# Optimization experiments

Measured on AMD Instinct MI355X. Metric: run time of the kernel, lower is better.

Reference implementation:

```python
import jax, jax.numpy as jnp
import numpy as np

D_MODEL = 1024
N_HEADS = 16
D_K = D_MODEL // N_HEADS


def _glorot(key, fan_in, fan_out):
    limit = np.sqrt(6.0 / (fan_in + fan_out)).astype(np.float32)
    return jax.random.uniform(key, (fan_in, fan_out), jnp.float32, -limit, limit)


def setup_inputs() -> dict:
    key = jax.random.key(0)
    kx, kq, kk, kv = jax.random.split(key, 4)
    x = jax.random.normal(kx, (2, 2048, D_MODEL), jnp.float32)
    Wq = _glorot(kq, D_MODEL, D_MODEL)
    Wk = _glorot(kk, D_MODEL, D_MODEL)
    Wv = _glorot(kv, D_MODEL, D_MODEL)
    bq = jnp.zeros((D_MODEL,), jnp.float32)
    bk = jnp.zeros((D_MODEL,), jnp.float32)
    bv = jnp.zeros((D_MODEL,), jnp.float32)
    return {"x": x, "Wq": Wq, "bq": bq, "Wk": Wk, "bk": bk, "Wv": Wv, "bv": bv}


def reference(x, Wq, bq, Wk, bk, Wv, bv):
    B, S, _ = x.shape
    # QKV projections (Dense layers with bias)
    q = (x @ Wq + bq).reshape(B, S, N_HEADS, D_K).transpose(0, 2, 1, 3)  # [B,H,S,Dk]
    k = (x @ Wk + bk).reshape(B, S, N_HEADS, D_K).transpose(0, 2, 1, 3)
    v = (x @ Wv + bv).reshape(B, S, N_HEADS, D_K).transpose(0, 2, 1, 3)
    # raw exp-based softmax (NO max subtraction, per original module)
    scores = jnp.einsum('bhqd,bhkd->bhqk', q, k) / np.sqrt(D_K).astype(np.float32)
    scores = jnp.exp(scores)
    attn = scores / (jnp.sum(scores, axis=-1, keepdims=True) + 1e-8)
    context = jnp.einsum('bhqk,bhkd->bhqd', attn, v)  # [B,H,S,Dk]
    return context.transpose(0, 2, 1, 3).reshape(B, S, N_HEADS * D_K)
```

## Files before the change

### kernel.cpp

```cpp
#include <hip/hip_runtime.h>
#include <hip/hip_bf16.h>
#include <stdint.h>

typedef __bf16 bf16x8 __attribute__((ext_vector_type(8)));
typedef __bf16 bf16x4 __attribute__((ext_vector_type(4)));
typedef float  f32x4  __attribute__((ext_vector_type(4)));
typedef short  s16x4  __attribute__((ext_vector_type(4)));
typedef unsigned short u16_t;

#define MFMA(a, b, c)   __builtin_amdgcn_mfma_f32_16x16x32_bf16((a), (b), (c), 0, 0, 0)
#define MFMA16(a, b, c) __builtin_amdgcn_mfma_f32_16x16x16bf16_1k((a), (b), (c), 0, 0, 0)

__device__ __forceinline__ void cp16(const void* g, void* l) {
  __builtin_amdgcn_global_load_lds(
      (const __attribute__((address_space(1))) unsigned int*)g,
      (__attribute__((address_space(3))) unsigned int*)l, 16, 0, 0);
}

__global__ __launch_bounds__(256) void k_prep(const float* __restrict__ x,
                                              const float* __restrict__ W0,
                                              const float* __restrict__ W1,
                                              const float* __restrict__ W2,
                                              u16_t* __restrict__ xb,
                                              u16_t* __restrict__ Wt) {
  __shared__ u16_t T[64][65];
  int bx = blockIdx.x, t = threadIdx.x;
  if (bx < 4096) {
    int i = bx * 256 + t;
    float4 f = ((const float4*)x)[i];
    bf16x4 o = {(__bf16)f.x, (__bf16)f.y, (__bf16)f.z, (__bf16)f.w};
    *(bf16x4*)&xb[(size_t)i * 4] = o;
    return;
  }
  int j = bx - 4096;
  int nx = j & 15, ny = (j >> 4) & 15, z = j >> 8;
  const float* W = z == 0 ? W0 : (z == 1 ? W1 : W2);
  int k0 = ny * 64, n0 = nx * 64;
#pragma unroll
  for (int i = 0; i < 16; i++) {
    int e = i * 256 + t, r = e >> 6, c = e & 63;
    __bf16 hv = (__bf16)W[(size_t)(k0 + r) * 1024 + n0 + c];
    T[r][c] = *(u16_t*)&hv;
  }
  __syncthreads();
  size_t base = ((size_t)z * 1024 + n0) * 1024 + k0;
#pragma unroll
  for (int i = 0; i < 16; i++) {
    int e = i * 256 + t, r = e >> 6, c = e & 63;
    Wt[base + (size_t)r * 1024 + c] = T[c][r];
  }
}

__global__ __launch_bounds__(256) void k_gemm_qkv(
    const u16_t* __restrict__ A, const u16_t* __restrict__ Bt,
    const float* __restrict__ bq, const float* __restrict__ bk,
    const float* __restrict__ bv,
    u16_t* __restrict__ Qo, u16_t* __restrict__ Ko, u16_t* __restrict__ Vo) {
  __shared__ u16_t As[128 * 32];
  __shared__ u16_t Bs[128 * 32];
  const int tid = threadIdx.x, lane = tid & 63, wv = tid >> 6;
  const int quad = lane >> 4, col = lane & 15;
  const int wm = wv >> 1, wn = wv & 1;
  const int tn = blockIdx.x * 128, tm = blockIdx.y * 128;
  f32x4 acc[4][4] = {};

  const int c0 = wv * 2;
  const int srow = lane >> 2;
  const int spc = lane & 3;

  for (int kk = 0; kk < 1024; kk += 32) {
#pragma unroll
    for (int i = 0; i < 2; i++) {
      int c = c0 + i;
      int m = c * 16 + srow;
      int lch = spc ^ ((m >> 1) & 3);
      cp16(A + (size_t)(tm + m) * 1024 + kk + lch * 8, As + c * 512 + lane * 8);
      cp16(Bt + (size_t)(tn + m) * 1024 + kk + lch * 8, Bs + c * 512 + lane * 8);
    }
    __syncthreads();
    bf16x8 af[4], bfv[4];
#pragma unroll
    for (int mt = 0; mt < 4; mt++) {
      int row = wm * 64 + mt * 16 + col;
      af[mt] = *(const bf16x8*)&As[row * 32 + (quad ^ ((row >> 1) & 3)) * 8];
    }
#pragma unroll
    for (int nt = 0; nt < 4; nt++) {
      int row = wn * 64 + nt * 16 + col;
      bfv[nt] = *(const bf16x8*)&Bs[row * 32 + (quad ^ ((row >> 1) & 3)) * 8];
    }
#pragma unroll
    for (int mt = 0; mt < 4; mt++)
#pragma unroll
      for (int nt = 0; nt < 4; nt++)
        acc[mt][nt] = MFMA(af[mt], bfv[nt], acc[mt][nt]);
    __syncthreads();
  }

  const int mat = tn >> 10;
  const float* bias = mat == 0 ? bq : (mat == 1 ? bk : bv);
  if (mat == 2) {
#pragma unroll
    for (int nt = 0; nt < 4; nt++) {
      int gn = tn + wn * 64 + nt * 16 + col;
      int d = gn & 1023, h = d >> 6, dk = d & 63;
      float bb = bias[d];
#pragma unroll
      for (int mt = 0; mt < 4; mt++) {
        int gm = tm + wm * 64 + mt * 16 + quad * 4;
        int b = gm >> 11, s = gm & 2047;
        bf16x4 pk4;
#pragma unroll
        for (int r = 0; r < 4; r++) pk4[r] = (__bf16)(acc[mt][nt][r] + bb);
        *(bf16x4*)&Vo[((size_t)((b * 16 + h) * 64 + dk)) * 2048 + s] = pk4;
      }
    }
  } else {
    u16_t* O = mat == 0 ? Qo : Ko;
    const float scl = mat == 0 ? 0.18033688011112042f : 1.0f;
#pragma unroll
    for (int nt = 0; nt < 4; nt++) {
      int gn = tn + wn * 64 + nt * 16 + col;
      int d = gn & 1023, h = d >> 6, dk = d & 63;
      float bb = bias[d];
#pragma unroll
      for (int mt = 0; mt < 4; mt++) {
#pragma unroll
        for (int r = 0; r < 4; r++) {
          int gm = tm + wm * 64 + mt * 16 + quad * 4 + r;
          int b = gm >> 11, s = gm & 2047;
          __bf16 hv = (__bf16)((acc[mt][nt][r] + bb) * scl);
          O[((size_t)((b * 16 + h) * 2048 + s)) * 64 + dk] = *(u16_t*)&hv;
        }
      }
    }
  }
}

__global__ __launch_bounds__(256, 4) void k_attn(const u16_t* __restrict__ Q,
                                                 const u16_t* __restrict__ K,
                                                 const u16_t* __restrict__ Vt,
                                                 float* __restrict__ out) {
  __shared__ u16_t smem[20480];
  u16_t* Qs  = smem;
  u16_t* Ksb = smem + 4096;
  u16_t* Vsb = smem + 12288;
  const int tid = threadIdx.x, lane = tid & 63, wv = tid >> 6;
  const int quad = lane >> 4, col = lane & 15;
  const int qh = wv >> 1, kh = wv & 1;
  const int qt = blockIdx.x, bh = blockIdx.y;
  const int b = bh >> 4, h = bh & 15;
  const int r8 = lane >> 3, c8 = lane & 7;

  const u16_t* Qg = Q + ((size_t)bh * 2048 + qt * 64) * 64;
  const u16_t* Kg = K + (size_t)bh * 2048 * 64;
  const u16_t* Vg = Vt + (size_t)bh * 64 * 2048;

#pragma unroll
  for (int i = 0; i < 2; i++) {
    int c = wv * 2 + i;
    int row = c * 8 + r8;
    int lch = c8 ^ r8;
    cp16(Qg + (size_t)row * 64 + lch * 8, Qs + c * 512 + lane * 8);
    cp16(Kg + (size_t)row * 64 + lch * 8, Ksb + c * 512 + lane * 8);
    cp16(Vg + (size_t)row * 2048 + lch * 8, Vsb + c * 512 + lane * 8);
  }
  __syncthreads();

  bf16x8 qf[2][2];
#pragma unroll
  for (int nt = 0; nt < 2; nt++)
#pragma unroll
    for (int ks = 0; ks < 2; ks++) {
      int row = qh * 32 + nt * 16 + col;
      qf[nt][ks] = *(const bf16x8*)&Qs[row * 64 + (((ks * 4 + quad) ^ (row & 7)) * 8)];
    }

  const short one_bf = (short)0x3F80;
  s16x4 ones4 = {one_bf, one_bf, one_bf, one_bf};

  f32x4 ao[2][4] = {};
  f32x4 dn[2] = {};

  for (int kt = 0; kt < 32; kt++) {
    const int cur = kt & 1;
    const u16_t* Kc = Ksb + cur * 4096;
    const u16_t* Vc = Vsb + cur * 4096;
    if (kt + 1 < 32) {
      u16_t* Kn = Ksb + (cur ^ 1) * 4096;
      u16_t* Vn = Vsb + (cur ^ 1) * 4096;
#pragma unroll
      for (int i = 0; i < 2; i++) {
        int c = wv * 2 + i;
        int row = c * 8 + r8;
        int lch = c8 ^ r8;
        cp16(Kg + (size_t)(kt + 1) * 4096 + (size_t)row * 64 + lch * 8,
             Kn + c * 512 + lane * 8);
        cp16(Vg + (size_t)row * 2048 + (kt + 1) * 64 + lch * 8,
             Vn + c * 512 + lane * 8);
      }
    }

    f32x4 sc[2][2] = {};
#pragma unroll
    for (int ks = 0; ks < 2; ks++) {
      bf16x8 kf[2];
#pragma unroll
      for (int mt = 0; mt < 2; mt++) {
        int row = kh * 32 + mt * 16 + col;
        kf[mt] = *(const bf16x8*)&Kc[row * 64 + (((ks * 4 + quad) ^ (row & 7)) * 8)];
      }
#pragma unroll
      for (int mt = 0; mt < 2; mt++)
#pragma unroll
        for (int nt = 0; nt < 2; nt++)
          sc[mt][nt] = MFMA(kf[mt], qf[nt][ks], sc[mt][nt]);
    }

    s16x4 pf[2][2];
#pragma unroll
    for (int mt = 0; mt < 2; mt++)
#pragma unroll
      for (int nt = 0; nt < 2; nt++) {
#pragma unroll
        for (int r = 0; r < 4; r++) {
          __bf16 e = (__bf16)__builtin_amdgcn_exp2f(sc[mt][nt][r]);
          pf[mt][nt][r] = *(short*)&e;
        }
        dn[nt] = MFMA16(pf[mt][nt], ones4, dn[nt]);
      }

#pragma unroll
    for (int mt = 0; mt < 2; mt++) {
#pragma unroll
      for (int dt = 0; dt < 4; dt++) {
        int row = dt * 16 + col;
        int c = kh * 4 + mt * 2 + (quad >> 1);
        int addr = row * 64 + ((c ^ (row & 7)) * 8) + (quad & 1) * 4;
        s16x4 vf = *(const s16x4*)&Vc[addr];
#pragma unroll
        for (int nt = 0; nt < 2; nt++)
          ao[nt][dt] = MFMA16(pf[mt][nt], vf, ao[nt][dt]);
      }
    }
    __syncthreads();
  }

  float* red = (float*)(smem + 4096);
  const int rb = (qh * 64 + lane) * 41;
  if (kh == 1) {
#pragma unroll
    for (int nt = 0; nt < 2; nt++) {
#pragma unroll
      for (int dt = 0; dt < 4; dt++)
#pragma unroll
        for (int r = 0; r < 4; r++)
          red[rb + (nt * 4 + dt) * 4 + r] = ao[nt][dt][r];
#pragma unroll
      for (int r = 0; r < 4; r++)
        red[rb + 32 + nt * 4 + r] = dn[nt][r];
    }
  }
  __syncthreads();
  if (kh == 0) {
#pragma unroll
    for (int nt = 0; nt < 2; nt++) {
      float dsum[4];
#pragma unroll
      for (int r = 0; r < 4; r++)
        dsum[r] = dn[nt][r] + red[rb + 32 + nt * 4 + r] + 1e-8f;
#pragma unroll
      for (int dt = 0; dt < 4; dt++) {
#pragma unroll
        for (int r = 0; r < 4; r++) {
          float v = (ao[nt][dt][r] + red[rb + (nt * 4 + dt) * 4 + r]) / dsum[r];
          int s = qt * 64 + qh * 32 + nt * 16 + quad * 4 + r;
          out[((size_t)b * 2048 + s) * 1024 + h * 64 + dt * 16 + col] = v;
        }
      }
    }
  }
}

extern "C" void kernel_launch(void* const* d_in, const int* in_sizes, int n_in,
                              void* d_out, int out_size, void* d_ws, size_t ws_size,
                              hipStream_t stream) {
  const float* x  = (const float*)d_in[0];
  const float* Wq = (const float*)d_in[1];
  const float* bq = (const float*)d_in[2];
  const float* Wk = (const float*)d_in[3];
  const float* bk = (const float*)d_in[4];
  const float* Wv = (const float*)d_in[5];
  const float* bv = (const float*)d_in[6];
  float* out = (float*)d_out;

  char* ws = (char*)d_ws;
  u16_t* xb  = (u16_t*)(ws);
  u16_t* Wt  = (u16_t*)(ws + 8388608);
  u16_t* Qb  = (u16_t*)(ws + 14680064);
  u16_t* Kb  = (u16_t*)(ws + 23068672);
  u16_t* Vtb = (u16_t*)(ws + 31457280);

  hipLaunchKernelGGL(k_prep, dim3(4864), dim3(256), 0, stream, x, Wq, Wk, Wv, xb, Wt);
  hipLaunchKernelGGL(k_gemm_qkv, dim3(24, 32), dim3(256), 0, stream,
                     xb, Wt, bq, bk, bv, Qb, Kb, Vtb);
  hipLaunchKernelGGL(k_attn, dim3(32, 32), dim3(256), 0, stream, Qb, Kb, Vtb, out);
}
```

Before: 170.7 us.

## Shrink attention blocks to 32 queries with two waves and smaller KV tiles

The attention kernel now uses 128-thread blocks, each handling 32 query rows with two waves that split each 32-key tile, instead of 256-thread blocks handling 64 queries. The grid doubles to 2048 blocks and LDS per block drops to 16 KB. Q fragments are loaded straight from global memory rather than staged through LDS, and the K/V tiles are half-sized with a new swizzle. The aim is more blocks and waves resident per CU and better load balance. In exchange, every K/V tile is read from global memory by twice as many blocks, and there are twice as many loop iterations and barriers.

```diff
diff --git a/kernel.cpp b/kernel.cpp
--- a/kernel.cpp
+++ b/kernel.cpp
@@ -137,44 +137,38 @@
   }
 }
 
-__global__ __launch_bounds__(256, 4) void k_attn(const u16_t* __restrict__ Q,
+__global__ __launch_bounds__(128, 4) void k_attn(const u16_t* __restrict__ Q,
                                                  const u16_t* __restrict__ K,
                                                  const u16_t* __restrict__ Vt,
                                                  float* __restrict__ out) {
-  __shared__ u16_t smem[20480];
-  u16_t* Qs  = smem;
-  u16_t* Ksb = smem + 4096;
-  u16_t* Vsb = smem + 12288;
-  const int tid = threadIdx.x, lane = tid & 63, wv = tid >> 6;
+  __shared__ u16_t smem[8192];
+  u16_t* Ksb = smem;
+  u16_t* Vsb = smem + 4096;
+  const int tid = threadIdx.x, lane = tid & 63, kh = tid >> 6;
   const int quad = lane >> 4, col = lane & 15;
-  const int qh = wv >> 1, kh = wv & 1;
   const int qt = blockIdx.x, bh = blockIdx.y;
   const int b = bh >> 4, h = bh & 15;
-  const int r8 = lane >> 3, c8 = lane & 7;
-
-  const u16_t* Qg = Q + ((size_t)bh * 2048 + qt * 64) * 64;
+
+  const u16_t* Qg = Q + ((size_t)bh * 2048 + qt * 32) * 64;
   const u16_t* Kg = K + (size_t)bh * 2048 * 64;
   const u16_t* Vg = Vt + (size_t)bh * 64 * 2048;
 
-#pragma unroll
-  for (int i = 0; i < 2; i++) {
-    int c = wv * 2 + i;
-    int row = c * 8 + r8;
-    int lch = c8 ^ r8;
-    cp16(Qg + (size_t)row * 64 + lch * 8, Qs + c * 512 + lane * 8);
-    cp16(Kg + (size_t)row * 64 + lch * 8, Ksb + c * 512 + lane * 8);
-    cp16(Vg + (size_t)row * 2048 + lch * 8, Vsb + c * 512 + lane * 8);
-  }
-  __syncthreads();
+  const int krow = lane >> 3, kch = (lane & 7) ^ (lane >> 3);
+  const int vrow = lane >> 2, vch = (lane & 3) ^ ((lane >> 3) & 3);
+
+#pragma unroll
+  for (int j = 0; j < 2; j++) {
+    int sl = kh * 2 + j;
+    cp16(Kg + (size_t)(sl * 8 + krow) * 64 + kch * 8, Ksb + sl * 512 + lane * 8);
+    cp16(Vg + (size_t)(sl * 16 + vrow) * 2048 + vch * 8, Vsb + sl * 512 + lane * 8);
+  }
 
   bf16x8 qf[2][2];
 #pragma unroll
   for (int nt = 0; nt < 2; nt++)
 #pragma unroll
-    for (int ks = 0; ks < 2; ks++) {
-      int row = qh * 32 + nt * 16 + col;
-      qf[nt][ks] = *(const bf16x8*)&Qs[row * 64 + (((ks * 4 + quad) ^ (row & 7)) * 8)];
-    }
+    for (int ks = 0; ks < 2; ks++)
+      qf[nt][ks] = *(const bf16x8*)&Qg[(size_t)(nt * 16 + col) * 64 + ks * 32 + quad * 8];
 
   const short one_bf = (short)0x3F80;
   s16x4 ones4 = {one_bf, one_bf, one_bf, one_bf};
@@ -182,72 +176,60 @@
   f32x4 ao[2][4] = {};
   f32x4 dn[2] = {};
 
-  for (int kt = 0; kt < 32; kt++) {
+  const int vpch = (kh * 2 + (quad >> 1)) ^ ((col >> 1) & 3);
+  __syncthreads();
+
+  for (int kt = 0; kt < 64; kt++) {
     const int cur = kt & 1;
-    const u16_t* Kc = Ksb + cur * 4096;
-    const u16_t* Vc = Vsb + cur * 4096;
-    if (kt + 1 < 32) {
-      u16_t* Kn = Ksb + (cur ^ 1) * 4096;
-      u16_t* Vn = Vsb + (cur ^ 1) * 4096;
-#pragma unroll
-      for (int i = 0; i < 2; i++) {
-        int c = wv * 2 + i;
-        int row = c * 8 + r8;
-        int lch = c8 ^ r8;
-        cp16(Kg + (size_t)(kt + 1) * 4096 + (size_t)row * 64 + lch * 8,
-             Kn + c * 512 + lane * 8);
-        cp16(Vg + (size_t)row * 2048 + (kt + 1) * 64 + lch * 8,
-             Vn + c * 512 + lane * 8);
-      }
-    }
-
-    f32x4 sc[2][2] = {};
+    const u16_t* Kc = Ksb + cur * 2048;
+    const u16_t* Vc = Vsb + cur * 2048;
+    if (kt + 1 < 64) {
+      u16_t* Kn = Ksb + (cur ^ 1) * 2048;
+      u16_t* Vn = Vsb + (cur ^ 1) * 2048;
+#pragma unroll
+      for (int j = 0; j < 2; j++) {
+        int sl = kh * 2 + j;
+        cp16(Kg + (size_t)((kt + 1) * 32 + sl * 8 + krow) * 64 + kch * 8,
+             Kn + sl * 512 + lane * 8);
+        cp16(Vg + (size_t)(sl * 16 + vrow) * 2048 + (kt + 1) * 32 + vch * 8,
+             Vn + sl * 512 + lane * 8);
+      }
+    }
+
+    f32x4 sc[2] = {};
 #pragma unroll
     for (int ks = 0; ks < 2; ks++) {
-      bf16x8 kf[2];
-#pragma unroll
-      for (int mt = 0; mt < 2; mt++) {
-        int row = kh * 32 + mt * 16 + col;
-        kf[mt] = *(const bf16x8*)&Kc[row * 64 + (((ks * 4 + quad) ^ (row & 7)) * 8)];
-      }
-#pragma unroll
-      for (int mt = 0; mt < 2; mt++)
-#pragma unroll
-        for (int nt = 0; nt < 2; nt++)
-          sc[mt][nt] = MFMA(kf[mt], qf[nt][ks], sc[mt][nt]);
-    }
-
-    s16x4 pf[2][2];
-#pragma unroll
-    for (int mt = 0; mt < 2; mt++)
-#pragma unroll
-      for (int nt = 0; nt < 2; nt++) {
-#pragma unroll
-        for (int r = 0; r < 4; r++) {
-          __bf16 e = (__bf16)__builtin_amdgcn_exp2f(sc[mt][nt][r]);
-          pf[mt][nt][r] = *(short*)&e;
-        }
-        dn[nt] = MFMA16(pf[mt][nt], ones4, dn[nt]);
-      }
-
-#pragma unroll
-    for (int mt = 0; mt < 2; mt++) {
-#pragma unroll
-      for (int dt = 0; dt < 4; dt++) {
-        int row = dt * 16 + col;
-        int c = kh * 4 + mt * 2 + (quad >> 1);
-        int addr = row * 64 + ((c ^ (row & 7)) * 8) + (quad & 1) * 4;
-        s16x4 vf = *(const s16x4*)&Vc[addr];
-#pragma unroll
-        for (int nt = 0; nt < 2; nt++)
-          ao[nt][dt] = MFMA16(pf[mt][nt], vf, ao[nt][dt]);
-      }
+      int row = kh * 16 + col;
+      bf16x8 kf = *(const bf16x8*)&Kc[row * 64 + (((ks * 4 + quad) ^ (col & 7)) * 8)];
+#pragma unroll
+      for (int nt = 0; nt < 2; nt++)
+        sc[nt] = MFMA(kf, qf[nt][ks], sc[nt]);
+    }
+
+    s16x4 pf[2];
+#pragma unroll
+    for (int nt = 0; nt < 2; nt++) {
+#pragma unroll
+      for (int r = 0; r < 4; r++) {
+        __bf16 e = (__bf16)__builtin_amdgcn_exp2f(sc[nt][r]);
+        pf[nt][r] = *(short*)&e;
+      }
+      dn[nt] = MFMA16(pf[nt], ones4, dn[nt]);
+    }
+
+#pragma unroll
+    for (int dt = 0; dt < 4; dt++) {
+      int d = dt * 16 + col;
+      s16x4 vf = *(const s16x4*)&Vc[d * 32 + vpch * 8 + (quad & 1) * 4];
+#pragma unroll
+      for (int nt = 0; nt < 2; nt++)
+        ao[nt][dt] = MFMA16(pf[nt], vf, ao[nt][dt]);
     }
     __syncthreads();
   }
 
-  float* red = (float*)(smem + 4096);
-  const int rb = (qh * 64 + lane) * 41;
+  float* red = (float*)smem;
+  const int rb = lane * 41;
   if (kh == 1) {
 #pragma unroll
     for (int nt = 0; nt < 2; nt++) {
@@ -274,7 +256,7 @@
 #pragma unroll
         for (int r = 0; r < 4; r++) {
           float v = (ao[nt][dt][r] + red[rb + (nt * 4 + dt) * 4 + r]) / dsum[r];
-          int s = qt * 64 + qh * 32 + nt * 16 + quad * 4 + r;
+          int s = qt * 32 + nt * 16 + quad * 4 + r;
           out[((size_t)b * 2048 + s) * 1024 + h * 64 + dt * 16 + col] = v;
         }
       }
@@ -304,5 +286,5 @@
   hipLaunchKernelGGL(k_prep, dim3(4864), dim3(256), 0, stream, x, Wq, Wk, Wv, xb, Wt);
   hipLaunchKernelGGL(k_gemm_qkv, dim3(24, 32), dim3(256), 0, stream,
                      xb, Wt, bq, bk, bv, Qb, Kb, Vtb);
-  hipLaunchKernelGGL(k_attn, dim3(32, 32), dim3(256), 0, stream, Qb, Kb, Vtb, out);
-}
+  hipLaunchKernelGGL(k_attn, dim3(64, 32), dim3(128), 0, stream, Qb, Kb, Vtb, out);
+}
```

Result: slower. 184.0 us (+7.8%).

## Restructure attention into two-wave blocks with per-wave private K/V pipelines

Applied to the files above, without the earlier changes.

The attention kernel now uses 128-thread blocks with two waves. Each wave covers all 64 query rows and half of the key range (1024 keys), and streams its own K/V tiles into private LDS double buffers. This removes the block-wide __syncthreads inside the key loop, replacing it with explicit vmcnt waits. Q fragments are loaded straight from global memory into registers, the grid is flattened with a remapped block index for L2 locality, and the V tile layout and swizzle change to 32-key tiles. The cost is more accumulator registers per wave (4x4 output tiles) and a lower occupancy target, and the correctness of the per-wave LDS reuse relies on the waitcnt reasoning.

```diff
diff --git a/kernel.cpp b/kernel.cpp
--- a/kernel.cpp
+++ b/kernel.cpp
@@ -137,91 +137,88 @@
   }
 }
 
-__global__ __launch_bounds__(256, 4) void k_attn(const u16_t* __restrict__ Q,
+__global__ __launch_bounds__(128, 3) void k_attn(const u16_t* __restrict__ Q,
                                                  const u16_t* __restrict__ K,
                                                  const u16_t* __restrict__ Vt,
                                                  float* __restrict__ out) {
-  __shared__ u16_t smem[20480];
-  u16_t* Qs  = smem;
-  u16_t* Ksb = smem + 4096;
-  u16_t* Vsb = smem + 12288;
-  const int tid = threadIdx.x, lane = tid & 63, wv = tid >> 6;
+  __shared__ u16_t smem[16384];
+  const int tid = threadIdx.x, lane = tid & 63, kh = tid >> 6;
   const int quad = lane >> 4, col = lane & 15;
-  const int qh = wv >> 1, kh = wv & 1;
-  const int qt = blockIdx.x, bh = blockIdx.y;
+
+  const int bid = blockIdx.x;
+  const int bh = (bid & 7) + 8 * ((bid >> 3) >> 5);
+  const int qt = (bid >> 3) & 31;
   const int b = bh >> 4, h = bh & 15;
-  const int r8 = lane >> 3, c8 = lane & 7;
-
+
+  u16_t* wbase = smem + kh * 8192;
   const u16_t* Qg = Q + ((size_t)bh * 2048 + qt * 64) * 64;
-  const u16_t* Kg = K + (size_t)bh * 2048 * 64;
-  const u16_t* Vg = Vt + (size_t)bh * 64 * 2048;
-
-#pragma unroll
-  for (int i = 0; i < 2; i++) {
-    int c = wv * 2 + i;
-    int row = c * 8 + r8;
-    int lch = c8 ^ r8;
-    cp16(Qg + (size_t)row * 64 + lch * 8, Qs + c * 512 + lane * 8);
-    cp16(Kg + (size_t)row * 64 + lch * 8, Ksb + c * 512 + lane * 8);
-    cp16(Vg + (size_t)row * 2048 + lch * 8, Vsb + c * 512 + lane * 8);
-  }
-  __syncthreads();
-
-  bf16x8 qf[2][2];
-#pragma unroll
-  for (int nt = 0; nt < 2; nt++)
-#pragma unroll
-    for (int ks = 0; ks < 2; ks++) {
-      int row = qh * 32 + nt * 16 + col;
-      qf[nt][ks] = *(const bf16x8*)&Qs[row * 64 + (((ks * 4 + quad) ^ (row & 7)) * 8)];
-    }
+  const u16_t* Kg = K + ((size_t)bh * 2048 + kh * 1024) * 64;
+  const u16_t* Vg = Vt + (size_t)bh * 64 * 2048 + kh * 1024;
+
+  bf16x8 qf[4][2];
+#pragma unroll
+  for (int nt = 0; nt < 4; nt++)
+#pragma unroll
+    for (int ks = 0; ks < 2; ks++)
+      qf[nt][ks] = *(const bf16x8*)&Qg[(size_t)(nt * 16 + col) * 64 + ks * 32 + quad * 8];
+
+  const int kr = lane >> 3, kc = (lane & 7) ^ (lane >> 3);
+  const int vr = lane >> 2, vc = (lane & 3) ^ ((lane >> 3) & 3);
+
+#pragma unroll
+  for (int sl = 0; sl < 4; sl++) {
+    cp16(Kg + (size_t)(sl * 8 + kr) * 64 + kc * 8, wbase + sl * 512 + lane * 8);
+    cp16(Vg + (size_t)(sl * 16 + vr) * 2048 + vc * 8, wbase + 4096 + sl * 512 + lane * 8);
+  }
 
   const short one_bf = (short)0x3F80;
   s16x4 ones4 = {one_bf, one_bf, one_bf, one_bf};
 
-  f32x4 ao[2][4] = {};
-  f32x4 dn[2] = {};
-
+  f32x4 ao[4][4] = {};
+  f32x4 dn[4] = {};
+
+#pragma unroll 2
   for (int kt = 0; kt < 32; kt++) {
     const int cur = kt & 1;
-    const u16_t* Kc = Ksb + cur * 4096;
-    const u16_t* Vc = Vsb + cur * 4096;
+    u16_t* Kb = wbase + cur * 2048;
+    u16_t* Vb = wbase + 4096 + cur * 2048;
+
     if (kt + 1 < 32) {
-      u16_t* Kn = Ksb + (cur ^ 1) * 4096;
-      u16_t* Vn = Vsb + (cur ^ 1) * 4096;
-#pragma unroll
-      for (int i = 0; i < 2; i++) {
-        int c = wv * 2 + i;
-        int row = c * 8 + r8;
-        int lch = c8 ^ r8;
-        cp16(Kg + (size_t)(kt + 1) * 4096 + (size_t)row * 64 + lch * 8,
-             Kn + c * 512 + lane * 8);
-        cp16(Vg + (size_t)row * 2048 + (kt + 1) * 64 + lch * 8,
-             Vn + c * 512 + lane * 8);
-      }
-    }
-
-    f32x4 sc[2][2] = {};
+      u16_t* Kn = wbase + (cur ^ 1) * 2048;
+      u16_t* Vn = wbase + 4096 + (cur ^ 1) * 2048;
+#pragma unroll
+      for (int sl = 0; sl < 4; sl++) {
+        cp16(Kg + (size_t)((kt + 1) * 32 + sl * 8 + kr) * 64 + kc * 8,
+             Kn + sl * 512 + lane * 8);
+        cp16(Vg + (size_t)(sl * 16 + vr) * 2048 + (kt + 1) * 32 + vc * 8,
+             Vn + sl * 512 + lane * 8);
+      }
+      asm volatile("s_waitcnt vmcnt(8)" ::: "memory");
+    } else {
+      asm volatile("s_waitcnt vmcnt(0)" ::: "memory");
+    }
+
+    f32x4 sc[2][4] = {};
 #pragma unroll
     for (int ks = 0; ks < 2; ks++) {
       bf16x8 kf[2];
 #pragma unroll
       for (int mt = 0; mt < 2; mt++) {
-        int row = kh * 32 + mt * 16 + col;
-        kf[mt] = *(const bf16x8*)&Kc[row * 64 + (((ks * 4 + quad) ^ (row & 7)) * 8)];
+        int row = mt * 16 + col;
+        kf[mt] = *(const bf16x8*)&Kb[row * 64 + (((ks * 4 + quad) ^ (row & 7)) * 8)];
       }
 #pragma unroll
       for (int mt = 0; mt < 2; mt++)
 #pragma unroll
-        for (int nt = 0; nt < 2; nt++)
+        for (int nt = 0; nt < 4; nt++)
           sc[mt][nt] = MFMA(kf[mt], qf[nt][ks], sc[mt][nt]);
     }
 
-    s16x4 pf[2][2];
+    s16x4 pf[2][4];
 #pragma unroll
     for (int mt = 0; mt < 2; mt++)
 #pragma unroll
-      for (int nt = 0; nt < 2; nt++) {
+      for (int nt = 0; nt < 4; nt++) {
 #pragma unroll
         for (int r = 0; r < 4; r++) {
           __bf16 e = (__bf16)__builtin_amdgcn_exp2f(sc[mt][nt][r]);
@@ -234,23 +231,22 @@
     for (int mt = 0; mt < 2; mt++) {
 #pragma unroll
       for (int dt = 0; dt < 4; dt++) {
-        int row = dt * 16 + col;
-        int c = kh * 4 + mt * 2 + (quad >> 1);
-        int addr = row * 64 + ((c ^ (row & 7)) * 8) + (quad & 1) * 4;
-        s16x4 vf = *(const s16x4*)&Vc[addr];
-#pragma unroll
-        for (int nt = 0; nt < 2; nt++)
+        int d = dt * 16 + col;
+        int phys = (mt * 2 + (quad >> 1)) ^ ((col >> 1) & 3);
+        s16x4 vf = *(const s16x4*)&Vb[d * 32 + phys * 8 + (quad & 1) * 4];
+#pragma unroll
+        for (int nt = 0; nt < 4; nt++)
           ao[nt][dt] = MFMA16(pf[mt][nt], vf, ao[nt][dt]);
       }
     }
-    __syncthreads();
-  }
-
-  float* red = (float*)(smem + 4096);
-  const int rb = (qh * 64 + lane) * 41;
+  }
+
+  float* red = (float*)smem;
+  const int rb = lane * 81;
+  __syncthreads();
   if (kh == 1) {
 #pragma unroll
-    for (int nt = 0; nt < 2; nt++) {
+    for (int nt = 0; nt < 4; nt++) {
 #pragma unroll
       for (int dt = 0; dt < 4; dt++)
 #pragma unroll
@@ -258,23 +254,23 @@
           red[rb + (nt * 4 + dt) * 4 + r] = ao[nt][dt][r];
 #pragma unroll
       for (int r = 0; r < 4; r++)
-        red[rb + 32 + nt * 4 + r] = dn[nt][r];
+        red[rb + 64 + nt * 4 + r] = dn[nt][r];
     }
   }
   __syncthreads();
   if (kh == 0) {
 #pragma unroll
-    for (int nt = 0; nt < 2; nt++) {
+    for (int nt = 0; nt < 4; nt++) {
       float dsum[4];
 #pragma unroll
       for (int r = 0; r < 4; r++)
-        dsum[r] = dn[nt][r] + red[rb + 32 + nt * 4 + r] + 1e-8f;
+        dsum[r] = dn[nt][r] + red[rb + 64 + nt * 4 + r] + 1e-8f;
 #pragma unroll
       for (int dt = 0; dt < 4; dt++) {
 #pragma unroll
         for (int r = 0; r < 4; r++) {
           float v = (ao[nt][dt][r] + red[rb + (nt * 4 + dt) * 4 + r]) / dsum[r];
-          int s = qt * 64 + qh * 32 + nt * 16 + quad * 4 + r;
+          int s = qt * 64 + nt * 16 + quad * 4 + r;
           out[((size_t)b * 2048 + s) * 1024 + h * 64 + dt * 16 + col] = v;
         }
       }
@@ -304,5 +300,5 @@
   hipLaunchKernelGGL(k_prep, dim3(4864), dim3(256), 0, stream, x, Wq, Wk, Wv, xb, Wt);
   hipLaunchKernelGGL(k_gemm_qkv, dim3(24, 32), dim3(256), 0, stream,
                      xb, Wt, bq, bk, bv, Qb, Kb, Vtb);
-  hipLaunchKernelGGL(k_attn, dim3(32, 32), dim3(256), 0, stream, Qb, Kb, Vtb, out);
-}
+  hipLaunchKernelGGL(k_attn, dim3(1024), dim3(128), 0, stream, Qb, Kb, Vtb, out);
+}
```

New measurement: 184.2 us. 7.9% more time.

## Deepen QKV GEMM K-tile to 64, remap attention blocks, unroll key loop

Applied to the files above, without the earlier changes.

The QKV projection GEMM now stages 64-wide K slices per iteration instead of 32, using an XOR swizzle over 8 chunks. This halves the number of barrier pairs and the load-issue overhead, at the cost of twice the LDS per block, and it adds an occupancy hint of 4 blocks per CU. The attention kernel moves to a 1D grid that interleaves 8 batch-heads across consecutive blocks, changing which blocks share L2 data. It also unrolls the key-tile loop by 2, which may raise register pressure.

```diff
diff --git a/kernel.cpp b/kernel.cpp
--- a/kernel.cpp
+++ b/kernel.cpp
@@ -51,49 +51,50 @@
   }
 }
 
-__global__ __launch_bounds__(256) void k_gemm_qkv(
+__global__ __launch_bounds__(256, 4) void k_gemm_qkv(
     const u16_t* __restrict__ A, const u16_t* __restrict__ Bt,
     const float* __restrict__ bq, const float* __restrict__ bk,
     const float* __restrict__ bv,
     u16_t* __restrict__ Qo, u16_t* __restrict__ Ko, u16_t* __restrict__ Vo) {
-  __shared__ u16_t As[128 * 32];
-  __shared__ u16_t Bs[128 * 32];
+  __shared__ u16_t As[128 * 64];
+  __shared__ u16_t Bs[128 * 64];
   const int tid = threadIdx.x, lane = tid & 63, wv = tid >> 6;
   const int quad = lane >> 4, col = lane & 15;
   const int wm = wv >> 1, wn = wv & 1;
   const int tn = blockIdx.x * 128, tm = blockIdx.y * 128;
   f32x4 acc[4][4] = {};
 
-  const int c0 = wv * 2;
-  const int srow = lane >> 2;
-  const int spc = lane & 3;
-
-  for (int kk = 0; kk < 1024; kk += 32) {
-#pragma unroll
-    for (int i = 0; i < 2; i++) {
-      int c = c0 + i;
-      int m = c * 16 + srow;
-      int lch = spc ^ ((m >> 1) & 3);
-      cp16(A + (size_t)(tm + m) * 1024 + kk + lch * 8, As + c * 512 + lane * 8);
-      cp16(Bt + (size_t)(tn + m) * 1024 + kk + lch * 8, Bs + c * 512 + lane * 8);
+  const int r8 = lane >> 3, c8 = lane & 7;
+  const int lch = c8 ^ r8;
+
+  for (int kk = 0; kk < 1024; kk += 64) {
+#pragma unroll
+    for (int i = 0; i < 4; i++) {
+      int blk = wv * 4 + i;
+      int m = blk * 8 + r8;
+      cp16(A + (size_t)(tm + m) * 1024 + kk + lch * 8, As + blk * 512 + lane * 8);
+      cp16(Bt + (size_t)(tn + m) * 1024 + kk + lch * 8, Bs + blk * 512 + lane * 8);
     }
     __syncthreads();
-    bf16x8 af[4], bfv[4];
-#pragma unroll
-    for (int mt = 0; mt < 4; mt++) {
-      int row = wm * 64 + mt * 16 + col;
-      af[mt] = *(const bf16x8*)&As[row * 32 + (quad ^ ((row >> 1) & 3)) * 8];
-    }
-#pragma unroll
-    for (int nt = 0; nt < 4; nt++) {
-      int row = wn * 64 + nt * 16 + col;
-      bfv[nt] = *(const bf16x8*)&Bs[row * 32 + (quad ^ ((row >> 1) & 3)) * 8];
-    }
-#pragma unroll
-    for (int mt = 0; mt < 4; mt++)
-#pragma unroll
-      for (int nt = 0; nt < 4; nt++)
-        acc[mt][nt] = MFMA(af[mt], bfv[nt], acc[mt][nt]);
+#pragma unroll
+    for (int ks = 0; ks < 2; ks++) {
+      bf16x8 af[4], bfv[4];
+#pragma unroll
+      for (int mt = 0; mt < 4; mt++) {
+        int row = wm * 64 + mt * 16 + col;
+        af[mt] = *(const bf16x8*)&As[row * 64 + (((ks * 4 + quad) ^ (row & 7)) * 8)];
+      }
+#pragma unroll
+      for (int nt = 0; nt < 4; nt++) {
+        int row = wn * 64 + nt * 16 + col;
+        bfv[nt] = *(const bf16x8*)&Bs[row * 64 + (((ks * 4 + quad) ^ (row & 7)) * 8)];
+      }
+#pragma unroll
+      for (int mt = 0; mt < 4; mt++)
+#pragma unroll
+        for (int nt = 0; nt < 4; nt++)
+          acc[mt][nt] = MFMA(af[mt], bfv[nt], acc[mt][nt]);
+    }
     __syncthreads();
   }
 
@@ -148,7 +149,10 @@
   const int tid = threadIdx.x, lane = tid & 63, wv = tid >> 6;
   const int quad = lane >> 4, col = lane & 15;
   const int qh = wv >> 1, kh = wv & 1;
-  const int qt = blockIdx.x, bh = blockIdx.y;
+
+  const int bid = blockIdx.x;
+  const int bh = (bid & 7) + 8 * ((bid >> 3) >> 5);
+  const int qt = (bid >> 3) & 31;
   const int b = bh >> 4, h = bh & 15;
   const int r8 = lane >> 3, c8 = lane & 7;
 
@@ -182,6 +186,7 @@
   f32x4 ao[2][4] = {};
   f32x4 dn[2] = {};
 
+#pragma unroll 2
   for (int kt = 0; kt < 32; kt++) {
     const int cur = kt & 1;
     const u16_t* Kc = Ksb + cur * 4096;
@@ -304,5 +309,5 @@
   hipLaunchKernelGGL(k_prep, dim3(4864), dim3(256), 0, stream, x, Wq, Wk, Wv, xb, Wt);
   hipLaunchKernelGGL(k_gemm_qkv, dim3(24, 32), dim3(256), 0, stream,
                      xb, Wt, bq, bk, bv, Qb, Kb, Vtb);
-  hipLaunchKernelGGL(k_attn, dim3(32, 32), dim3(256), 0, stream, Qb, Kb, Vtb, out);
-}
+  hipLaunchKernelGGL(k_attn, dim3(1024), dim3(256), 0, stream, Qb, Kb, Vtb, out);
+}
```

After: 168.3 us. No clear change (-1.4%).
